# Optimization experiments

Hardware: AMD Instinct MI355X
Metric: run time of the kernel (lower is better)

## Reference

```python
import jax, jax.numpy as jnp
import numpy as np

B, S, H, NH, HD = 2, 2048, 1024, 16, 64
RD = 16            # rotary_dim = head_dim * 0.25
W = 16             # mini_context_length (sliding window)
SCALE = HD ** -0.5
ROPE_BASE = 10000.0


def setup_inputs() -> dict:
    key = jax.random.key(0)
    ks = jax.random.split(key, 10)
    p = lambda k, shape: (jax.random.normal(k, shape, dtype=jnp.float32) * 0.02)
    return {
        "hidden_states": jax.random.normal(ks[0], (B, S, H), dtype=jnp.float32),
        "Wqkv": p(ks[1], (3 * H, H)), "bqkv": p(ks[2], (3 * H,)),
        "Wqa": p(ks[3], (H, H)),      "bqa": p(ks[4], (H,)),
        "Wka": p(ks[5], (H, H)),      "bka": p(ks[6], (H,)),
        "Wd": p(ks[7], (H, H)),       "bd": p(ks[8], (H,)),
    }


def _rotate_half(x):
    x1, x2 = jnp.split(x, 2, axis=-1)
    return jnp.concatenate([-x2, x1], axis=-1)


def _apply_rope(q, k, seq_len):
    # GPT-NeoX style rotary on the first RD dims. q,k: [B,NH,S,RD]
    inv_freq = 1.0 / (ROPE_BASE ** (jnp.arange(0, RD, 2, dtype=jnp.float32) / RD))
    t = jnp.arange(seq_len, dtype=jnp.float32)
    freqs = jnp.outer(t, inv_freq)                     # [S, RD//2]
    emb = jnp.concatenate([freqs, freqs], axis=-1)     # [S, RD]
    cos = jnp.cos(emb)[None, None]                      # [1,1,S,RD]
    sin = jnp.sin(emb)[None, None]
    return q * cos + _rotate_half(q) * sin, k * cos + _rotate_half(k) * sin


def reference(hidden_states, Wqkv, bqkv, Wqa, bqa, Wka, bka, Wd, bd):
    b, s, _ = hidden_states.shape
    qkv = hidden_states @ Wqkv.T + bqkv                       # [B,S,3H]
    qkv = qkv.reshape(b, s, 3, NH, HD).transpose(2, 0, 3, 1, 4)
    q, k, v = qkv[0], qkv[1], qkv[2]                          # [B,NH,S,HD]

    q_rot, k_rot = _apply_rope(q[..., :RD], k[..., :RD], s)
    q = jnp.concatenate([q_rot, q[..., RD:]], axis=-1)
    k = jnp.concatenate([k_rot, k[..., RD:]], axis=-1)

    # ----- Stage 1: sliding-window local attention (vectorized) -----
    pos = jnp.arange(s)
    idx = pos[:, None] - (W - 1) + jnp.arange(W)[None, :]     # [S,W]
    valid = idx >= 0
    idxc = jnp.clip(idx, 0, s - 1)
    k_win = k[:, :, idxc, :]                                   # [B,NH,S,W,HD]
    v_win = v[:, :, idxc, :]
    scores = jnp.einsum('bhsd,bhswd->bhsw', q, k_win) * SCALE
    scores = jnp.where(valid[None, None], scores, -jnp.inf)
    probs = jax.nn.softmax(scores, axis=-1)
    A = jnp.einsum('bhsw,bhswd->bhsd', probs, v_win)           # [B,NH,S,HD]

    A_hidden = A.transpose(0, 2, 1, 3).reshape(b, s, H)        # [B,S,H]

    # ----- Stage 2: causal global attention over A -----
    qa = (A_hidden @ Wqa.T + bqa).reshape(b, s, NH, HD).transpose(0, 2, 1, 3)
    ka = (A_hidden @ Wka.T + bka).reshape(b, s, NH, HD).transpose(0, 2, 1, 3)
    g = jnp.einsum('bhqd,bhkd->bhqk', qa, ka) * SCALE          # [B,NH,S,S]
    causal = pos[:, None] >= pos[None, :]
    g = jnp.where(causal[None, None], g, -jnp.inf)
    pg = jax.nn.softmax(g, axis=-1)
    out = jnp.einsum('bhqk,bhkd->bhqd', pg, A)                 # [B,NH,S,HD]
    out = out.transpose(0, 2, 1, 3).reshape(b, s, H)
    return out @ Wd.T + bd
```

## Files before the change

### kernel.cpp

```cpp
#include <hip/hip_runtime.h>
#include <hip/hip_bf16.h>
#include <cstdint>
#include <cstddef>

typedef __bf16 bf16;
typedef __bf16 bf16x4 __attribute__((ext_vector_type(4)));
typedef __bf16 bf16x8 __attribute__((ext_vector_type(8)));
typedef float  f32x4  __attribute__((ext_vector_type(4)));

#define DEVINL __device__ __forceinline__

constexpr int   Bc  = 2, Sc = 2048, Hc = 1024, NHc = 16, HDc = 64;
constexpr int   Tc  = Bc * Sc;
constexpr float L2E = 1.44269504088896340736f;
constexpr float NEG_BIG = -1.0e30f;

typedef __attribute__((address_space(1))) void AS1void;
typedef __attribute__((address_space(3))) void AS3void;

DEVINL void load_lds16(const bf16* g, bf16* l) {
  __builtin_amdgcn_global_load_lds((AS1void*)g, (AS3void*)l, 16, 0, 0);
}


__global__ __launch_bounds__(256)
void convert_all(const float* __restrict__ hs, const float* __restrict__ Wqkv,
                 const float* __restrict__ Wqa, const float* __restrict__ Wka,
                 const float* __restrict__ Wd, const float* __restrict__ bqa,
                 const float* __restrict__ bka,
                 bf16* __restrict__ hsb, bf16* __restrict__ wqkvb,
                 bf16* __restrict__ wqakab, bf16* __restrict__ wdb,
                 float* __restrict__ bqaka) {
  const int blk = blockIdx.x;
  if (blk >= 5120) {
    const int i = threadIdx.x * 8;
    const float* src = (i < 1024) ? (bqa + i) : (bka + i - 1024);
    *(f32x4*)(bqaka + i)     = *(const f32x4*)src;
    *(f32x4*)(bqaka + i + 4) = *(const f32x4*)(src + 4);
    return;
  }
  const float* src; bf16* dst; int base;
  if      (blk < 2048) { src = hs;   dst = hsb;                    base = blk; }
  else if (blk < 3584) { src = Wqkv; dst = wqkvb;                  base = blk - 2048; }
  else if (blk < 4096) { src = Wqa;  dst = wqakab;                 base = blk - 3584; }
  else if (blk < 4608) { src = Wka;  dst = wqakab + 1024 * 1024;   base = blk - 4096; }
  else                 { src = Wd;   dst = wdb;                    base = blk - 4608; }
  const int i = (base * 256 + threadIdx.x) * 8;
  f32x4 a = *(const f32x4*)(src + i);
  f32x4 b = *(const f32x4*)(src + i + 4);
  bf16x8 v;
#pragma unroll
  for (int j = 0; j < 4; j++) { v[j] = (bf16)a[j]; v[4 + j] = (bf16)b[j]; }
  *(bf16x8*)(dst + i) = v;
}

template <typename CT>
__global__ __launch_bounds__(256, 3)
void gemm128(const bf16* __restrict__ A, const bf16* __restrict__ Bw,
             const float* __restrict__ bias, CT* __restrict__ C,
             int M, int N, int K) {
  __shared__ __attribute__((aligned(16))) bf16 As[128 * 64];
  __shared__ __attribute__((aligned(16))) bf16 Bs[128 * 64];

  const int tid = threadIdx.x, wv = tid >> 6, lane = tid & 63;
  const int m0 = blockIdx.y * 128, n0 = blockIdx.x * 128;
  const int col = lane & 15, quad = lane >> 4;
  const int wrow = (wv >> 1) * 64, wcol = (wv & 1) * 64;

  f32x4 acc[4][4];
#pragma unroll
  for (int i = 0; i < 4; i++)
#pragma unroll
    for (int j = 0; j < 4; j++) acc[i][j] = f32x4{0.f, 0.f, 0.f, 0.f};

  const int srow = tid >> 3;
  const int scol = (((tid & 7) ^ (srow & 7)) << 3);
  const bf16* Ag = A  + (size_t)(m0 + srow) * K + scol;
  const bf16* Bg = Bw + (size_t)(n0 + srow) * K + scol;
  const int cs = col & 7;

  for (int k0 = 0; k0 < K; k0 += 64) {
#pragma unroll
    for (int c = 0; c < 4; c++) {
      load_lds16(Ag + (size_t)(c * 32) * K + k0, As + c * 2048 + tid * 8);
      load_lds16(Bg + (size_t)(c * 32) * K + k0, Bs + c * 2048 + tid * 8);
    }
    __syncthreads();
#pragma unroll
    for (int kk = 0; kk < 64; kk += 32) {
      const int so = ((((kk >> 3) + quad) ^ cs) << 3);
      bf16x8 af[4], bfr[4];
#pragma unroll
      for (int i = 0; i < 4; i++)
        af[i] = *(const bf16x8*)(As + (wrow + i * 16 + col) * 64 + so);
#pragma unroll
      for (int j = 0; j < 4; j++)
        bfr[j] = *(const bf16x8*)(Bs + (wcol + j * 16 + col) * 64 + so);
#pragma unroll
      for (int i = 0; i < 4; i++)
#pragma unroll
        for (int j = 0; j < 4; j++)
          acc[i][j] = __builtin_amdgcn_mfma_f32_16x16x32_bf16(af[i], bfr[j], acc[i][j], 0, 0, 0);
    }
    __syncthreads();
  }

#pragma unroll
  for (int j = 0; j < 4; j++) {
    const int c = n0 + wcol + j * 16 + col;
    const float bv = bias[c];
#pragma unroll
    for (int i = 0; i < 4; i++)
#pragma unroll
      for (int r = 0; r < 4; r++) {
        const int rr = m0 + wrow + i * 16 + quad * 4 + r;
        C[(size_t)rr * N + c] = (CT)(acc[i][j][r] + bv);
      }
  }
}

template <typename CT>
__global__ __launch_bounds__(256, 4)
void gemm6464(const bf16* __restrict__ A, const bf16* __restrict__ Bw,
              const float* __restrict__ bias, CT* __restrict__ C,
              int M, int N, int K) {
  __shared__ __attribute__((aligned(16))) bf16 As[64 * 64];
  __shared__ __attribute__((aligned(16))) bf16 Bs[64 * 64];

  const int tid = threadIdx.x, wv = tid >> 6, lane = tid & 63;
  const int m0 = blockIdx.y * 64, n0 = blockIdx.x * 64;
  const int col = lane & 15, quad = lane >> 4;

  f32x4 acc[4];
#pragma unroll
  for (int j = 0; j < 4; j++) acc[j] = f32x4{0.f, 0.f, 0.f, 0.f};

  const int srow = tid >> 3;
  const int scol = (((tid & 7) ^ (srow & 7)) << 3);
  const bf16* Ag = A  + (size_t)(m0 + srow) * K + scol;
  const bf16* Bg = Bw + (size_t)(n0 + srow) * K + scol;
  const int cs = col & 7;

  for (int k0 = 0; k0 < K; k0 += 64) {
#pragma unroll
    for (int c = 0; c < 2; c++) {
      load_lds16(Ag + (size_t)(c * 32) * K + k0, As + c * 2048 + tid * 8);
      load_lds16(Bg + (size_t)(c * 32) * K + k0, Bs + c * 2048 + tid * 8);
    }
    __syncthreads();
#pragma unroll
    for (int kk = 0; kk < 64; kk += 32) {
      const int so = ((((kk >> 3) + quad) ^ cs) << 3);
      bf16x8 af = *(const bf16x8*)(As + (wv * 16 + col) * 64 + so);
#pragma unroll
      for (int j = 0; j < 4; j++) {
        bf16x8 bfr = *(const bf16x8*)(Bs + (j * 16 + col) * 64 + so);
        acc[j] = __builtin_amdgcn_mfma_f32_16x16x32_bf16(af, bfr, acc[j], 0, 0, 0);
      }
    }
    __syncthreads();
  }

#pragma unroll
  for (int j = 0; j < 4; j++) {
    const int c = n0 + j * 16 + col;
    const float bv = bias[c];
#pragma unroll
    for (int r = 0; r < 4; r++) {
      const int rr = m0 + wv * 16 + quad * 4 + r;
      C[(size_t)rr * N + c] = (CT)(acc[j][r] + bv);
    }
  }
}

__global__ __launch_bounds__(256)
void window_attn(const bf16* __restrict__ qkv, bf16* __restrict__ Ah,
                 bf16* __restrict__ VTg) {
  __shared__ __attribute__((aligned(16))) bf16 Kw[31 * 72];
  __shared__ __attribute__((aligned(16))) bf16 Vw[31 * 72];
  const int g  = blockIdx.x;
  const int st = g & 127;
  const int h  = (g >> 7) & 15;
  const int b  = g >> 11;
  const int s0 = st * 16;
  const int tid = threadIdx.x;

  if ((tid < 124) || (tid >= 128 && tid < 252)) {
    const bool isK = tid < 124;
    const int lt  = isK ? tid : tid - 128;
    const int r   = lt >> 2, off = (lt & 3) << 4;
    int sidx = s0 - 15 + r; if (sidx < 0) sidx = 0;
    const bf16* src = qkv + (size_t)(b * Sc + sidx) * 3072 + (isK ? 1024 : 2048) + h * 64 + off;
    bf16x8 v0 = *(const bf16x8*)src;
    bf16x8 v1 = *(const bf16x8*)(src + 8);
    if (isK && off == 0) {
#pragma unroll
      for (int j = 0; j < 8; j++) {
        const float invf = exp2f(-(float)j * 1.66096404744368128f);
        float sn, csn;
        sincosf((float)sidx * invf, &sn, &csn);
        const float x1 = (float)v0[j], x2 = (float)v1[j];
        v0[j] = (bf16)(x1 * csn - x2 * sn);
        v1[j] = (bf16)(x2 * csn + x1 * sn);
      }
    }
    bf16* dst = (isK ? Kw : Vw) + r * 72 + off;
    *(bf16x8*)dst       = v0;
    *(bf16x8*)(dst + 8) = v1;
  }
  __syncthreads();

  const int wv = tid >> 6, lane = tid & 63;
  const int subq = lane >> 4, lane16 = lane & 15;
  const int s = s0 + wv * 4 + subq;
  const int t = b * Sc + s;
  const int d0 = lane16 * 4;

  float qd[4];
  {
    bf16x4 qv = *(const bf16x4*)(qkv + (size_t)t * 3072 + h * 64 + d0);
#pragma unroll
    for (int j = 0; j < 4; j++) qd[j] = (float)qv[j];
  }
  float pd[4];
#pragma unroll
  for (int j = 0; j < 4; j++) pd[j] = __shfl_xor(qd[j], 2, 64);
  if (lane16 < 4) {
#pragma unroll
    for (int j = 0; j < 4; j++) {
      const int jabs = d0 + j;
      const float invf = exp2f(-(float)(jabs & 7) * 1.66096404744368128f);
      float sn, csn;
      sincosf((float)s * invf, &sn, &csn);
      qd[j] = (jabs < 8) ? (qd[j] * csn - pd[j] * sn) : (qd[j] * csn + pd[j] * sn);
    }
  }

  float sc[16];
#pragma unroll
  for (int w = 0; w < 16; w++) {
    const int idxp = s - 15 + w;
    const int row = idxp - s0 + 15;
    bf16x4 kv = *(const bf16x4*)(Kw + row * 72 + d0);
    float p = qd[0] * (float)kv[0] + qd[1] * (float)kv[1] +
              qd[2] * (float)kv[2] + qd[3] * (float)kv[3];
#pragma unroll
    for (int m = 1; m < 16; m <<= 1) p += __shfl_xor(p, m, 64);
    sc[w] = (idxp < 0) ? NEG_BIG : p * 0.125f;
  }
  float mx = sc[0];
#pragma unroll
  for (int w = 1; w < 16; w++) mx = fmaxf(mx, sc[w]);
  float sum = 0.f;
#pragma unroll
  for (int w = 0; w < 16; w++) { sc[w] = exp2f((sc[w] - mx) * L2E); sum += sc[w]; }
  const float inv = 1.0f / fmaxf(sum, 1e-30f);

  float acc[4] = {0.f, 0.f, 0.f, 0.f};
#pragma unroll
  for (int w = 0; w < 16; w++) {
    const int idxp = s - 15 + w;
    const int row = idxp - s0 + 15;
    bf16x4 vv = *(const bf16x4*)(Vw + row * 72 + d0);
#pragma unroll
    for (int j = 0; j < 4; j++) acc[j] += sc[w] * (float)vv[j];
  }
  bf16x4 ov;
#pragma unroll
  for (int j = 0; j < 4; j++) ov[j] = (bf16)(acc[j] * inv);
  *(bf16x4*)(Ah + (size_t)t * 1024 + h * 64 + d0) = ov;
  bf16* vt = VTg + (((size_t)(b * 16 + h)) * 64 + d0) * 2048 + s;
#pragma unroll
  for (int j = 0; j < 4; j++) vt[(size_t)j * 2048] = ov[j];
}

__global__ __launch_bounds__(256, 3)
void flash_attn(const bf16* __restrict__ Q, const bf16* __restrict__ Kt,
                const bf16* __restrict__ VTg, bf16* __restrict__ O) {
  constexpr int QS = 2048;
  constexpr float SHIFT = 16.0f;
  __shared__ __attribute__((aligned(16))) bf16 K_lds[128 * 64];
  __shared__ __attribute__((aligned(16))) bf16 VT_lds[64 * 128];
  __shared__ __attribute__((aligned(16))) bf16 P_lds[4][16 * 136];

  const int tid = threadIdx.x, wv = tid >> 6, lane = tid & 63;
  const int bh = blockIdx.x;
  const int y  = blockIdx.y;
  const int gq = y & 7, kq = y >> 3;
  const int qt = (kq == 0) ? gq : (kq == 1) ? (15 - gq)
               : (kq == 2) ? (16 + gq) : (31 - gq);
  const int b = bh >> 4, h = bh & 15;
  const int col = lane & 15, quad = lane >> 4;
  const size_t bS = (size_t)b * Sc;
  const int hd = h * 64;

  const int krow = tid >> 3;
  const int kcol = (((tid & 7) ^ (krow & 7)) << 3);
  const int vrow = tid >> 4;
  const int vcol = (((tid & 15) ^ vrow) << 3);
  const int cs8 = col & 7;

  const int qbase = qt * 64 + wv * 16;
  const int nkt = (qt + 2) >> 1;

  const bf16* qptr = Q + (bS + qbase + col) * QS + hd + quad * 8;
  bf16x8 qf[2];
  qf[0] = *(const bf16x8*)qptr;
  qf[1] = *(const bf16x8*)(qptr + 32);
#pragma unroll
  for (int hh = 0; hh < 2; hh++)
#pragma unroll
    for (int j = 0; j < 8; j++) qf[hh][j] = (bf16)((float)qf[hh][j] * 0.125f);

  f32x4 oacc[4];
#pragma unroll
  for (int i = 0; i < 4; i++) oacc[i] = f32x4{0.f, 0.f, 0.f, 0.f};
  float lrow[4] = {0.f, 0.f, 0.f, 0.f};

  for (int kt0 = 0; kt0 < nkt; kt0++) {
    const int k0 = kt0 * 128;
#pragma unroll
    for (int c = 0; c < 4; c++) {
      load_lds16(Kt + (bS + k0 + c * 32 + krow) * QS + hd + kcol,
                 K_lds + c * 2048 + tid * 8);
      load_lds16(VTg + ((size_t)bh * 64 + c * 16 + vrow) * 2048 + k0 + vcol,
                 VT_lds + c * 2048 + tid * 8);
    }
    __syncthreads();

    f32x4 sacc[8];
#pragma unroll
    for (int sub = 0; sub < 8; sub++) {
      f32x4 a = f32x4{0.f, 0.f, 0.f, 0.f};
#pragma unroll
      for (int hh = 0; hh < 2; hh++) {
        const int so = (((hh * 4 + quad) ^ cs8) << 3);
        bf16x8 kf = *(const bf16x8*)(K_lds + (sub * 16 + col) * 64 + so);
        a = __builtin_amdgcn_mfma_f32_16x16x32_bf16(qf[hh], kf, a, 0, 0, 0);
      }
      sacc[sub] = a;
    }
    if (kt0 == nkt - 1) {
#pragma unroll
      for (int sub = 0; sub < 8; sub++)
#pragma unroll
        for (int r = 0; r < 4; r++) {
          const int key = k0 + sub * 16 + col;
          const int qq  = qbase + quad * 4 + r;
          if (key > qq) sacc[sub][r] = NEG_BIG;
        }
    }
#pragma unroll
    for (int sub = 0; sub < 8; sub++)
#pragma unroll
      for (int r = 0; r < 4; r++)
        sacc[sub][r] = exp2f(sacc[sub][r] * L2E - SHIFT);
#pragma unroll
    for (int r = 0; r < 4; r++)
      lrow[r] += ((sacc[0][r] + sacc[1][r]) + (sacc[2][r] + sacc[3][r]))
               + ((sacc[4][r] + sacc[5][r]) + (sacc[6][r] + sacc[7][r]));
#pragma unroll
    for (int sub = 0; sub < 8; sub++)
#pragma unroll
      for (int r = 0; r < 4; r++)
        P_lds[wv][(quad * 4 + r) * 136 + sub * 16 + col] = (bf16)sacc[sub][r];
#pragma unroll
    for (int kk = 0; kk < 128; kk += 32) {
      bf16x8 pf = *(const bf16x8*)&P_lds[wv][col * 136 + kk + quad * 8];
      const int vso = ((((kk >> 3) + quad) ^ col) << 3);
#pragma unroll
      for (int nb = 0; nb < 4; nb++) {
        bf16x8 vf = *(const bf16x8*)(VT_lds + (nb * 16 + col) * 128 + vso);
        oacc[nb] = __builtin_amdgcn_mfma_f32_16x16x32_bf16(pf, vf, oacc[nb], 0, 0, 0);
      }
    }
    __syncthreads();
  }

#pragma unroll
  for (int m = 1; m < 16; m <<= 1)
#pragma unroll
    for (int r = 0; r < 4; r++) lrow[r] += __shfl_xor(lrow[r], m, 64);
#pragma unroll
  for (int r = 0; r < 4; r++) lrow[r] = 1.0f / fmaxf(lrow[r], 1e-37f);
#pragma unroll
  for (int nb = 0; nb < 4; nb++)
#pragma unroll
    for (int r = 0; r < 4; r++) {
      const int qq = qbase + quad * 4 + r;
      O[(bS + qq) * 1024 + hd + nb * 16 + col] = (bf16)(oacc[nb][r] * lrow[r]);
    }
}

extern "C" void kernel_launch(void* const* d_in, const int* in_sizes, int n_in,
                              void* d_out, int out_size, void* d_ws, size_t ws_size,
                              hipStream_t stream) {
  (void)in_sizes; (void)n_in; (void)out_size; (void)ws_size;
  const float* hs   = (const float*)d_in[0];
  const float* Wqkv = (const float*)d_in[1];
  const float* bqkv = (const float*)d_in[2];
  const float* Wqa  = (const float*)d_in[3];
  const float* bqa  = (const float*)d_in[4];
  const float* Wka  = (const float*)d_in[5];
  const float* bka  = (const float*)d_in[6];
  const float* Wd   = (const float*)d_in[7];
  const float* bd   = (const float*)d_in[8];
  float* out = (float*)d_out;

  const size_t TH = (size_t)Tc * Hc;
  bf16* dob   = (bf16*)d_out;
  bf16* hsb   = dob;
  bf16* wqkvb = dob + TH;
  bf16* Ah    = dob;
  bf16* VTg   = dob + TH;
  bf16* ws     = (bf16*)d_ws;
  bf16* qkv    = ws;
  bf16* qaka   = ws;
  bf16* oh     = ws + 2 * TH;
  bf16* wqakab = ws + 3 * TH;
  bf16* wdb    = wqakab + 2 * 1024 * 1024;
  float* bqaka = (float*)(wdb + 1024 * 1024);

  convert_all<<<dim3(5121), 256, 0, stream>>>(hs, Wqkv, Wqa, Wka, Wd, bqa, bka,
                                              hsb, wqkvb, wqakab, wdb, bqaka);

  gemm128<bf16><<<dim3(24, 32), 256, 0, stream>>>(hsb, wqkvb, bqkv, qkv, Tc, 3 * Hc, Hc);
  window_attn<<<dim3(Tc * NHc / 16), 256, 0, stream>>>(qkv, Ah, VTg);
  gemm128<bf16><<<dim3(16, 32), 256, 0, stream>>>(Ah, wqakab, bqaka, qaka, Tc, 2 * Hc, Hc);
  flash_attn<<<dim3(Bc * NHc, 32), 256, 0, stream>>>(qaka, qaka + Hc, VTg, oh);
  gemm6464<float><<<dim3(16, 64), 256, 0, stream>>>(oh, wdb, bd, out, Tc, Hc, Hc);
}
```

Before: 232.8 us.

## Compute transposed score tiles and pass P through bpermute instead of LDS

The flash attention kernel swaps the MFMA operand order so each lane holds scores for one query row across four keys. The probabilities are packed to bf16 pairs and reshuffled into the PV operand layout with ds_bpermute, which removes the per-wave P staging buffer in LDS and its write/read round trip. Row sums become a single scalar per lane reduced with two shuffles, and outputs are written as 4-wide vector stores. Launch bounds are raised to 4 blocks per CU to use the freed LDS, which risks register spills.

```diff
diff --git a/kernel.cpp b/kernel.cpp
--- a/kernel.cpp
+++ b/kernel.cpp
@@ -4,9 +4,11 @@
 #include <cstddef>
 
 typedef __bf16 bf16;
+typedef __bf16 bf16x2 __attribute__((ext_vector_type(2)));
 typedef __bf16 bf16x4 __attribute__((ext_vector_type(4)));
 typedef __bf16 bf16x8 __attribute__((ext_vector_type(8)));
 typedef float  f32x4  __attribute__((ext_vector_type(4)));
+typedef int    i32x4  __attribute__((ext_vector_type(4)));
 
 #define DEVINL __device__ __forceinline__
 
@@ -20,6 +22,12 @@
 
 DEVINL void load_lds16(const bf16* g, bf16* l) {
   __builtin_amdgcn_global_load_lds((AS1void*)g, (AS3void*)l, 16, 0, 0);
+}
+
+DEVINL int packbf(float a, float b) {
+  union { bf16x2 h; int i; } u;
+  u.h[0] = (bf16)a; u.h[1] = (bf16)b;
+  return u.i;
 }
 
 
@@ -274,14 +282,13 @@
   for (int j = 0; j < 4; j++) vt[(size_t)j * 2048] = ov[j];
 }
 
-__global__ __launch_bounds__(256, 3)
+__global__ __launch_bounds__(256, 4)
 void flash_attn(const bf16* __restrict__ Q, const bf16* __restrict__ Kt,
                 const bf16* __restrict__ VTg, bf16* __restrict__ O) {
   constexpr int QS = 2048;
   constexpr float SHIFT = 16.0f;
   __shared__ __attribute__((aligned(16))) bf16 K_lds[128 * 64];
   __shared__ __attribute__((aligned(16))) bf16 VT_lds[64 * 128];
-  __shared__ __attribute__((aligned(16))) bf16 P_lds[4][16 * 136];
 
   const int tid = threadIdx.x, wv = tid >> 6, lane = tid & 63;
   const int bh = blockIdx.x;
@@ -300,6 +307,9 @@
   const int vcol = (((tid & 15) ^ vrow) << 3);
   const int cs8 = col & 7;
 
+  const int idxA = (col + 16 * ((2 * quad) & 3)) << 2;
+  const int idxB = (col + 16 * ((2 * quad + 1) & 3)) << 2;
+
   const int qbase = qt * 64 + wv * 16;
   const int nkt = (qt + 2) >> 1;
 
@@ -315,7 +325,7 @@
   f32x4 oacc[4];
 #pragma unroll
   for (int i = 0; i < 4; i++) oacc[i] = f32x4{0.f, 0.f, 0.f, 0.f};
-  float lrow[4] = {0.f, 0.f, 0.f, 0.f};
+  float lsum = 0.f;
 
   for (int kt0 = 0; kt0 < nkt; kt0++) {
     const int k0 = kt0 * 128;
@@ -336,17 +346,17 @@
       for (int hh = 0; hh < 2; hh++) {
         const int so = (((hh * 4 + quad) ^ cs8) << 3);
         bf16x8 kf = *(const bf16x8*)(K_lds + (sub * 16 + col) * 64 + so);
-        a = __builtin_amdgcn_mfma_f32_16x16x32_bf16(qf[hh], kf, a, 0, 0, 0);
+        a = __builtin_amdgcn_mfma_f32_16x16x32_bf16(kf, qf[hh], a, 0, 0, 0);
       }
       sacc[sub] = a;
     }
     if (kt0 == nkt - 1) {
+      const int qq = qbase + col;
 #pragma unroll
       for (int sub = 0; sub < 8; sub++)
 #pragma unroll
         for (int r = 0; r < 4; r++) {
-          const int key = k0 + sub * 16 + col;
-          const int qq  = qbase + quad * 4 + r;
+          const int key = k0 + sub * 16 + quad * 4 + r;
           if (key > qq) sacc[sub][r] = NEG_BIG;
         }
     }
@@ -356,40 +366,61 @@
       for (int r = 0; r < 4; r++)
         sacc[sub][r] = exp2f(sacc[sub][r] * L2E - SHIFT);
 #pragma unroll
-    for (int r = 0; r < 4; r++)
-      lrow[r] += ((sacc[0][r] + sacc[1][r]) + (sacc[2][r] + sacc[3][r]))
-               + ((sacc[4][r] + sacc[5][r]) + (sacc[6][r] + sacc[7][r]));
-#pragma unroll
     for (int sub = 0; sub < 8; sub++)
-#pragma unroll
-      for (int r = 0; r < 4; r++)
-        P_lds[wv][(quad * 4 + r) * 136 + sub * 16 + col] = (bf16)sacc[sub][r];
-#pragma unroll
-    for (int kk = 0; kk < 128; kk += 32) {
-      bf16x8 pf = *(const bf16x8*)&P_lds[wv][col * 136 + kk + quad * 8];
-      const int vso = ((((kk >> 3) + quad) ^ col) << 3);
+      lsum += (sacc[sub][0] + sacc[sub][1]) + (sacc[sub][2] + sacc[sub][3]);
+    int pkl[8], pkh[8];
+#pragma unroll
+    for (int sub = 0; sub < 8; sub++) {
+      pkl[sub] = packbf(sacc[sub][0], sacc[sub][1]);
+      pkh[sub] = packbf(sacc[sub][2], sacc[sub][3]);
+    }
+#pragma unroll
+    for (int c = 0; c < 4; c++) {
+      const int sLo = 2 * c, sHi = 2 * c + 1;
+      i32x4 w;
+      {
+        int aL = __builtin_amdgcn_ds_bpermute(idxA, pkl[sLo]);
+        int aH = __builtin_amdgcn_ds_bpermute(idxA, pkl[sHi]);
+        w[0] = (quad < 2) ? aL : aH;
+      }
+      {
+        int aL = __builtin_amdgcn_ds_bpermute(idxA, pkh[sLo]);
+        int aH = __builtin_amdgcn_ds_bpermute(idxA, pkh[sHi]);
+        w[1] = (quad < 2) ? aL : aH;
+      }
+      {
+        int aL = __builtin_amdgcn_ds_bpermute(idxB, pkl[sLo]);
+        int aH = __builtin_amdgcn_ds_bpermute(idxB, pkl[sHi]);
+        w[2] = (quad < 2) ? aL : aH;
+      }
+      {
+        int aL = __builtin_amdgcn_ds_bpermute(idxB, pkh[sLo]);
+        int aH = __builtin_amdgcn_ds_bpermute(idxB, pkh[sHi]);
+        w[3] = (quad < 2) ? aL : aH;
+      }
+      union { i32x4 wi; bf16x8 v; } pb;
+      pb.wi = w;
+      const int vso = (((c * 4 + quad) ^ col) << 3);
 #pragma unroll
       for (int nb = 0; nb < 4; nb++) {
         bf16x8 vf = *(const bf16x8*)(VT_lds + (nb * 16 + col) * 128 + vso);
-        oacc[nb] = __builtin_amdgcn_mfma_f32_16x16x32_bf16(pf, vf, oacc[nb], 0, 0, 0);
-      }
-    }
-    __syncthreads();
-  }
-
-#pragma unroll
-  for (int m = 1; m < 16; m <<= 1)
-#pragma unroll
-    for (int r = 0; r < 4; r++) lrow[r] += __shfl_xor(lrow[r], m, 64);
-#pragma unroll
-  for (int r = 0; r < 4; r++) lrow[r] = 1.0f / fmaxf(lrow[r], 1e-37f);
-#pragma unroll
-  for (int nb = 0; nb < 4; nb++)
-#pragma unroll
-    for (int r = 0; r < 4; r++) {
-      const int qq = qbase + quad * 4 + r;
-      O[(bS + qq) * 1024 + hd + nb * 16 + col] = (bf16)(oacc[nb][r] * lrow[r]);
-    }
+        oacc[nb] = __builtin_amdgcn_mfma_f32_16x16x32_bf16(vf, pb.v, oacc[nb], 0, 0, 0);
+      }
+    }
+    __syncthreads();
+  }
+
+  lsum += __shfl_xor(lsum, 16, 64);
+  lsum += __shfl_xor(lsum, 32, 64);
+  const float inv = 1.0f / fmaxf(lsum, 1e-37f);
+  const int qq = qbase + col;
+#pragma unroll
+  for (int nb = 0; nb < 4; nb++) {
+    bf16x4 ov;
+#pragma unroll
+    for (int r = 0; r < 4; r++) ov[r] = (bf16)(oacc[nb][r] * inv);
+    *(bf16x4*)(O + (bS + qq) * 1024 + hd + nb * 16 + quad * 4) = ov;
+  }
 }
 
 extern "C" void kernel_launch(void* const* d_in, const int* in_sizes, int n_in,
```

New measurement: 240.8 us (median of 2 runs). +3.4%, slower.
